# Kernel tuning notes

Measured on AMD Instinct MI355X. Metric: run time of the kernel, lower is better.

Reference implementation:

```python
import jax, jax.numpy as jnp
import numpy as np

B, S, T, I, H = 256, 128, 64, 63, 1024


def setup_inputs() -> dict:
    key = jax.random.key(0)
    ks = jax.random.split(key, 12)
    sc = 1.0 / np.sqrt(H)

    def rn(k, shape, scale=1.0):
        return jax.random.normal(k, shape, dtype=jnp.float32) * scale

    return dict(
        encoder_inputs=rn(ks[0], (B, S, I)),
        decoder_inputs=rn(ks[1], (B, T, I)),
        # encoder GRU params (PyTorch layout: [3H, in], gate order r,z,n)
        enc_Wih=rn(ks[2], (3 * H, I), sc), enc_Whh=rn(ks[3], (3 * H, H), sc),
        enc_bih=rn(ks[4], (3 * H,), sc), enc_bhh=rn(ks[5], (3 * H,), sc),
        # decoder GRUCell params (input dim = I, see notes)
        dec_Wih=rn(ks[6], (3 * H, I), sc), dec_Whh=rn(ks[7], (3 * H, H), sc),
        dec_bih=rn(ks[8], (3 * H,), sc), dec_bhh=rn(ks[9], (3 * H,), sc),
        # projector Linear(H -> I)
        proj_W=rn(ks[10], (I, H), sc), proj_b=rn(ks[11], (I,), sc),
    )


def _gru_gates(gi, gh, h):
    # gi = W_ih x + b_ih, gh = W_hh h + b_hh; PyTorch gate order (r, z, n)
    i_r, i_z, i_n = jnp.split(gi, 3, axis=-1)
    h_r, h_z, h_n = jnp.split(gh, 3, axis=-1)
    r = jax.nn.sigmoid(i_r + h_r)
    z = jax.nn.sigmoid(i_z + h_z)
    n = jnp.tanh(i_n + r * h_n)
    return (1.0 - z) * n + z * h


def reference(encoder_inputs, decoder_inputs, enc_Wih, enc_Whh, enc_bih,
              enc_bhh, dec_Wih, dec_Whh, dec_bih, dec_bhh, proj_W, proj_b):
    hid = enc_Whh.shape[1]
    b = encoder_inputs.shape[0]
    # ---- encoder GRU (batch_first), input-side gates precomputed as one GEMM
    gi_all = jnp.einsum('bsi,gi->bsg', encoder_inputs, enc_Wih) + enc_bih  # (B,S,3H)

    def step(h, gi):
        gh = h @ enc_Whh.T + enc_bhh
        return _gru_gates(gi, gh, h), None

    h0 = jnp.zeros((b, hid), encoder_inputs.dtype)
    enc_h, _ = jax.lax.scan(step, h0, jnp.swapaxes(gi_all, 0, 1))  # (B,H) final hidden

    # ---- decoder: per the source, every timestep feeds the SAME encoder
    # hidden state into the GRUCell (state is not carried), so all timesteps
    # are independent and can be computed as batched GEMMs over (B,T).
    gi_dec = jnp.einsum('bti,gi->btg', decoder_inputs, dec_Wih) + dec_bih   # (B,T,3H)
    gh_dec = (enc_h @ dec_Whh.T + dec_bhh)[:, None, :]                       # (B,1,3H)
    next_states = _gru_gates(gi_dec, gh_dec, enc_h[:, None, :])              # (B,T,H)

    # dropout p=0.0 (identity); projector Linear
    outputs = jnp.einsum('bth,oh->bto', next_states, proj_W) + proj_b       # (B,T,I)
    return outputs
```

## Files before the change

### kernel.cpp

```cpp
#include <hip/hip_runtime.h>


typedef unsigned short u16;
typedef unsigned int   u32;
typedef __attribute__((ext_vector_type(8))) short s8v;
typedef __attribute__((ext_vector_type(4))) float f4v;
typedef __attribute__((ext_vector_type(4))) int  i4v;
typedef __attribute__((ext_vector_type(4))) unsigned int u4v;

__device__ __forceinline__ float b2f(u16 u) {
    return __uint_as_float(((u32)u) << 16);
}
__device__ __forceinline__ u16 f2b(float f) {
    u32 x = __float_as_uint(f);
    u32 r = x + 0x7fffu + ((x >> 16) & 1u);
    return (u16)(r >> 16);
}
__device__ __forceinline__ float sigf(float x) {
    return 1.0f / (1.0f + __expf(-x));
}
__device__ __forceinline__ f4v mfma16(s8v a, s8v b, f4v c) {
    return __builtin_amdgcn_mfma_f32_16x16x32_bf16(a, b, c, 0, 0, 0);
}
__device__ __forceinline__ void unpack8(u4v w0, u4v w1, s8v& hi, s8v& lo) {
    u32 c0 = w0[0], c1 = w0[1], c2 = w0[2], c3 = w0[3];
    u32 c4 = w1[0], c5 = w1[1], c6 = w1[2], c7 = w1[3];
    union { u32 u[4]; s8v v; } H, L;
    H.u[0] = (c0 & 0xffffu) | (c1 << 16);
    H.u[1] = (c2 & 0xffffu) | (c3 << 16);
    H.u[2] = (c4 & 0xffffu) | (c5 << 16);
    H.u[3] = (c6 & 0xffffu) | (c7 << 16);
    L.u[0] = (c0 >> 16) | (c1 & 0xffff0000u);
    L.u[1] = (c2 >> 16) | (c3 & 0xffff0000u);
    L.u[2] = (c4 >> 16) | (c5 & 0xffff0000u);
    L.u[3] = (c6 >> 16) | (c7 & 0xffff0000u);
    hi = H.v; lo = L.v;
}

__global__ void zero_ws(i4v* __restrict__ p, int n) {
    int i = blockIdx.x * blockDim.x + threadIdx.x;
    if (i < n) { i4v z = {0, 0, 0, 0}; p[i] = z; }
}

__global__ void conv_wih_split_pad(const float* __restrict__ s,
                                   u16* __restrict__ hi, u16* __restrict__ lo) {
    int idx = blockIdx.x * blockDim.x + threadIdx.x;
    int row = idx >> 6, col = idx & 63;
    float v = (col < 63) ? s[(size_t)row * 63 + col] : 0.f;
    u16 h = f2b(v);
    hi[idx] = h;
    lo[idx] = f2b(v - b2f(h));
}

__global__ void conv_pw_split_pad(const float* __restrict__ s,
                                  u16* __restrict__ hi, u16* __restrict__ lo) {
    int idx = blockIdx.x * blockDim.x + threadIdx.x;
    float v = (idx < 63 * 1024) ? s[idx] : 0.f;
    u16 h = f2b(v);
    hi[idx] = h;
    lo[idx] = f2b(v - b2f(h));
}

__global__ __launch_bounds__(512, 1) void enc_persist8(
    const float* __restrict__ Whh,
    const u16* __restrict__ WihH, const u16* __restrict__ WihL,
    const float* __restrict__ bih, const float* __restrict__ bhh,
    const float* __restrict__ xenc,
    u32* __restrict__ hbuf,
    int* __restrict__ ep)
{
    __shared__ f4v red[8][4][3][64];
    __shared__ u16 WisH[48 * 72];
    __shared__ u16 WisL[48 * 72];

    __builtin_amdgcn_fence(__ATOMIC_ACQUIRE, "agent");

    const int tid  = threadIdx.x;
    const int lane = tid & 63;
    const int wave = tid >> 6;
    const int lrow = lane & 15;
    const int lk8  = lane >> 4;
    const int bid = blockIdx.x;
    const int xcd = bid & 7;
    const int y   = bid >> 3;
    const int mt  = y & 3;
    const int jt  = xcd * 8 + (y >> 2);
    const int m0 = mt * 64;
    const int j0 = jt * 16;

    int* subCtr  = ep + (mt * 8 + xcd) * 16;
    int* waveCtr = ep + (mt * 8 + wave) * 16;

    if (tid < 192) {
        int wr = tid >> 2, qq = tid & 3;
        int grow = (wr >> 4) * 1024 + j0 + (wr & 15);
        const u16* wpH = WihH + (size_t)grow * 64 + qq * 16;
        const u16* wpL = WihL + (size_t)grow * 64 + qq * 16;
        *(i4v*)&WisH[wr * 72 + qq * 16]     = *(const i4v*)wpH;
        *(i4v*)&WisH[wr * 72 + qq * 16 + 8] = *(const i4v*)(wpH + 8);
        *(i4v*)&WisL[wr * 72 + qq * 16]     = *(const i4v*)wpL;
        *(i4v*)&WisL[wr * 72 + qq * 16 + 8] = *(const i4v*)(wpL + 8);
    }

    s8v bHf[3][4], bLf[3][4];
    const int k0 = wave * 128;
    #pragma unroll
    for (int gg = 0; gg < 3; ++gg)
        #pragma unroll
        for (int ks = 0; ks < 4; ++ks) {
            const float* p = Whh + (size_t)(gg * 1024 + j0 + lrow) * 1024 +
                             k0 + ks * 32 + lk8 * 8;
            f4v a = *(const f4v*)p;
            f4v b = *(const f4v*)(p + 4);
            union { u16 a[8]; s8v v; } H, L;
            #pragma unroll
            for (int j = 0; j < 8; ++j) {
                float v = (j < 4) ? a[j] : b[j - 4];
                u16 hh = f2b(v);
                H.a[j] = hh;
                L.a[j] = f2b(v - b2f(hh));
            }
            bHf[gg][ks] = H.v;
            bLf[gg][ks] = L.v;
        }

    const int jcol = j0 + lrow;
    const float bhr = bhh[jcol], bhz = bhh[1024 + jcol], bhn = bhh[2048 + jcol];
    const float bir = bih[jcol], biz = bih[1024 + jcol], bin = bih[2048 + jcol];

    size_t aoff[4];
    #pragma unroll
    for (int mtile = 0; mtile < 4; ++mtile)
        aoff[mtile] = (size_t)(m0 + mtile * 16 + lrow) * 1024 + k0 + lk8 * 8;

    const float* xrow = xenc + (size_t)(m0 + (wave & 3) * 16 + lrow) * 8064;
    float hprev[4] = {0.f, 0.f, 0.f, 0.f};

    float xf[16];
    if (wave < 4) {
        #pragma unroll
        for (int ks = 0; ks < 2; ++ks)
            #pragma unroll
            for (int j = 0; j < 8; ++j) {
                int col = ks * 32 + lk8 * 8 + j;
                xf[ks * 8 + j] = (col < 63) ? xrow[col] : 0.f;
            }
    }

    __syncthreads();

    for (int s = 0; s < 128; ++s) {
        const u32* hin = hbuf + (size_t)s * 262144;
        u32* hout      = hbuf + (size_t)(s + 1) * 262144;

        f4v gi_r = {0.f, 0.f, 0.f, 0.f};
        f4v gi_z = {0.f, 0.f, 0.f, 0.f};
        f4v gi_n = {0.f, 0.f, 0.f, 0.f};
        if (wave < 4) {
            #pragma unroll
            for (int ks = 0; ks < 2; ++ks) {
                union { u16 a[8]; s8v v; } xh, xl;
                #pragma unroll
                for (int j = 0; j < 8; ++j) {
                    float v = xf[ks * 8 + j];
                    u16 hh = f2b(v);
                    xh.a[j] = hh;
                    xl.a[j] = f2b(v - b2f(hh));
                }
                int ao = ks * 32 + lk8 * 8;
                s8v brh = *(const s8v*)&WisH[(lrow) * 72 + ao];
                s8v brl = *(const s8v*)&WisL[(lrow) * 72 + ao];
                s8v bzh = *(const s8v*)&WisH[(16 + lrow) * 72 + ao];
                s8v bzl = *(const s8v*)&WisL[(16 + lrow) * 72 + ao];
                s8v bnh = *(const s8v*)&WisH[(32 + lrow) * 72 + ao];
                s8v bnl = *(const s8v*)&WisL[(32 + lrow) * 72 + ao];
                gi_r = mfma16(xh.v, brh, gi_r);
                gi_r = mfma16(xh.v, brl, gi_r);
                gi_r = mfma16(xl.v, brh, gi_r);
                gi_z = mfma16(xh.v, bzh, gi_z);
                gi_z = mfma16(xh.v, bzl, gi_z);
                gi_z = mfma16(xl.v, bzh, gi_z);
                gi_n = mfma16(xh.v, bnh, gi_n);
                gi_n = mfma16(xh.v, bnl, gi_n);
                gi_n = mfma16(xl.v, bnh, gi_n);
            }
        }

        if (s) {
            const int tgt = s * 8;
            while (__hip_atomic_load(waveCtr, __ATOMIC_RELAXED,
                                     __HIP_MEMORY_SCOPE_SYSTEM) < tgt)
                __builtin_amdgcn_s_sleep(1);
        }

        f4v accr[4], accz[4], acchn[4];
        #pragma unroll
        for (int m = 0; m < 4; ++m) {
            accr[m]  = f4v{0.f, 0.f, 0.f, 0.f};
            accz[m]  = f4v{0.f, 0.f, 0.f, 0.f};
            acchn[m] = f4v{0.f, 0.f, 0.f, 0.f};
        }
        #pragma unroll
        for (int mtile = 0; mtile < 4; ++mtile) {
            #pragma unroll
            for (int ks = 0; ks < 4; ++ks) {
                const u32* p = hin + aoff[mtile] + ks * 32;
                u4v w0 = *(const u4v*)p;
                u4v w1 = *(const u4v*)(p + 4);
                s8v ahi, alo;
                unpack8(w0, w1, ahi, alo);
                accr[mtile]  = mfma16(ahi, bHf[0][ks], accr[mtile]);
                accr[mtile]  = mfma16(ahi, bLf[0][ks], accr[mtile]);
                accr[mtile]  = mfma16(alo, bHf[0][ks], accr[mtile]);
                accz[mtile]  = mfma16(ahi, bHf[1][ks], accz[mtile]);
                accz[mtile]  = mfma16(ahi, bLf[1][ks], accz[mtile]);
                accz[mtile]  = mfma16(alo, bHf[1][ks], accz[mtile]);
                acchn[mtile] = mfma16(ahi, bHf[2][ks], acchn[mtile]);
                acchn[mtile] = mfma16(ahi, bLf[2][ks], acchn[mtile]);
                acchn[mtile] = mfma16(alo, bHf[2][ks], acchn[mtile]);
            }
        }

        #pragma unroll
        for (int m = 0; m < 4; ++m) {
            red[wave][m][0][lane] = accr[m];
            red[wave][m][1][lane] = accz[m];
            red[wave][m][2][lane] = acchn[m];
        }
        __syncthreads();

        if (wave < 4) {
            f4v sr = {0.f, 0.f, 0.f, 0.f};
            f4v sz = {0.f, 0.f, 0.f, 0.f};
            f4v sh = {0.f, 0.f, 0.f, 0.f};
            #pragma unroll
            for (int w = 0; w < 8; ++w) {
                sr += red[w][wave][0][lane];
                sz += red[w][wave][1][lane];
                sh += red[w][wave][2][lane];
            }
            #pragma unroll
            for (int reg = 0; reg < 4; ++reg) {
                int brow = m0 + wave * 16 + lk8 * 4 + reg;
                float rr = sigf(sr[reg] + gi_r[reg] + bir + bhr);
                float zz = sigf(sz[reg] + gi_z[reg] + biz + bhz);
                float nn = tanhf(gi_n[reg] + bin + rr * (sh[reg] + bhn));
                float h = (1.f - zz) * nn + zz * hprev[reg];
                u16 hh = f2b(h);
                u16 ll = f2b(h - b2f(hh));
                hprev[reg] = b2f(hh) + b2f(ll);
                u32 pk = (u32)hh | ((u32)ll << 16);
                __hip_atomic_store(&hout[(size_t)brow * 1024 + jcol], pk,
                                   __ATOMIC_RELAXED, __HIP_MEMORY_SCOPE_SYSTEM);
            }
        }

        __syncthreads();
        if (tid == 0)
            __hip_atomic_fetch_add(subCtr, 1, __ATOMIC_RELAXED,
                                   __HIP_MEMORY_SCOPE_SYSTEM);
        if (wave < 4) {
            int sn = (s < 127) ? s + 1 : 127;
            const float* xr = xrow + sn * 63;
            #pragma unroll
            for (int ks = 0; ks < 2; ++ks)
                #pragma unroll
                for (int j = 0; j < 8; ++j) {
                    int col = ks * 32 + lk8 * 8 + j;
                    xf[ks * 8 + j] = (col < 63) ? xr[col] : 0.f;
                }
        }
    }
}

__global__ __launch_bounds__(256, 1) void gru_gemm1(
    const float* __restrict__ Whh,
    const float* __restrict__ bhh,
    const u32* __restrict__ hin,
    float* __restrict__ gh_out)
{
    __shared__ u16 WbH[48 * 264];
    __shared__ u16 WbL[48 * 264];

    const int tid  = threadIdx.x;
    const int lane = tid & 63;
    const int wave = tid >> 6;
    const int lrow = lane & 15;
    const int lk8  = lane >> 4;
    const int mt = blockIdx.x & 3;
    const int jt = blockIdx.x >> 2;
    const int m0 = mt * 64;
    const int j0 = jt * 16;

    f4v acc_r  = {0.f, 0.f, 0.f, 0.f};
    f4v acc_z  = {0.f, 0.f, 0.f, 0.f};
    f4v acc_hn = {0.f, 0.f, 0.f, 0.f};

    f4v stgA[6], stgB[6];
    #pragma unroll
    for (int i = 0; i < 6; ++i) {
        int c16 = i * 256 + tid;
        int row = c16 >> 5, p16 = c16 & 31;
        int grow = (row >> 4) * 1024 + j0 + (row & 15);
        const float* p = Whh + (size_t)grow * 1024 + p16 * 8;
        stgA[i] = *(const f4v*)p;
        stgB[i] = *(const f4v*)(p + 4);
    }
    #pragma unroll
    for (int i = 0; i < 6; ++i) {
        int c16 = i * 256 + tid;
        int row = c16 >> 5, p16 = c16 & 31;
        union { u16 a[8]; i4v v; } H, L;
        #pragma unroll
        for (int j = 0; j < 8; ++j) {
            float v = (j < 4) ? stgA[i][j] : stgB[i][j - 4];
            u16 hh = f2b(v);
            H.a[j] = hh;
            L.a[j] = f2b(v - b2f(hh));
        }
        *(i4v*)&WbH[row * 264 + p16 * 8] = H.v;
        *(i4v*)&WbL[row * 264 + p16 * 8] = L.v;
    }
    __syncthreads();

    const size_t arow = (size_t)(m0 + wave * 16 + lrow) * 1024 + lk8 * 8;
    const u32* hp = hin + arow;

    for (int c = 0; c < 4; ++c) {
        if (c < 3) {
            #pragma unroll
            for (int i = 0; i < 6; ++i) {
                int c16 = i * 256 + tid;
                int row = c16 >> 5, p16 = c16 & 31;
                int grow = (row >> 4) * 1024 + j0 + (row & 15);
                const float* p = Whh + (size_t)grow * 1024 + (c + 1) * 256 + p16 * 8;
                stgA[i] = *(const f4v*)p;
                stgB[i] = *(const f4v*)(p + 4);
            }
        }
        #pragma unroll
        for (int ks = 0; ks < 8; ++ks) {
            int kk = c * 256 + ks * 32;
            int bo = ks * 32 + lk8 * 8;
            u4v w0 = *(const u4v*)(hp + kk);
            u4v w1 = *(const u4v*)(hp + kk + 4);
            s8v ahi, alo;
            unpack8(w0, w1, ahi, alo);
            s8v brh = *(const s8v*)&WbH[(lrow) * 264 + bo];
            s8v brl = *(const s8v*)&WbL[(lrow) * 264 + bo];
            s8v bzh = *(const s8v*)&WbH[(16 + lrow) * 264 + bo];
            s8v bzl = *(const s8v*)&WbL[(16 + lrow) * 264 + bo];
            s8v bnh = *(const s8v*)&WbH[(32 + lrow) * 264 + bo];
            s8v bnl = *(const s8v*)&WbL[(32 + lrow) * 264 + bo];
            acc_r  = mfma16(ahi, brh, acc_r);
            acc_r  = mfma16(ahi, brl, acc_r);
            acc_r  = mfma16(alo, brh, acc_r);
            acc_z  = mfma16(ahi, bzh, acc_z);
            acc_z  = mfma16(ahi, bzl, acc_z);
            acc_z  = mfma16(alo, bzh, acc_z);
            acc_hn = mfma16(ahi, bnh, acc_hn);
            acc_hn = mfma16(ahi, bnl, acc_hn);
            acc_hn = mfma16(alo, bnh, acc_hn);
        }
        __syncthreads();
        if (c < 3) {
            #pragma unroll
            for (int i = 0; i < 6; ++i) {
                int c16 = i * 256 + tid;
                int row = c16 >> 5, p16 = c16 & 31;
                union { u16 a[8]; i4v v; } H, L;
                #pragma unroll
                for (int j = 0; j < 8; ++j) {
                    float v = (j < 4) ? stgA[i][j] : stgB[i][j - 4];
                    u16 hh = f2b(v);
                    H.a[j] = hh;
                    L.a[j] = f2b(v - b2f(hh));
                }
                *(i4v*)&WbH[row * 264 + p16 * 8] = H.v;
                *(i4v*)&WbL[row * 264 + p16 * 8] = L.v;
            }
            __syncthreads();
        }
    }

    const int jcol = j0 + lrow;
    const float bhr = bhh[jcol];
    const float bhz = bhh[1024 + jcol];
    const float bhn = bhh[2048 + jcol];
    #pragma unroll
    for (int reg = 0; reg < 4; ++reg) {
        int brow = m0 + wave * 16 + lk8 * 4 + reg;
        gh_out[(size_t)brow * 3072 + jcol]        = acc_r[reg] + bhr;
        gh_out[(size_t)brow * 3072 + 1024 + jcol] = acc_z[reg] + bhz;
        gh_out[(size_t)brow * 3072 + 2048 + jcol] = acc_hn[reg] + bhn;
    }
}

__global__ __launch_bounds__(256, 1) void dec_fused(
    const u16* __restrict__ WihH, const u16* __restrict__ WihL,
    const float* __restrict__ bih,
    const float* __restrict__ xdec,
    const u32* __restrict__ e32,
    const float* __restrict__ gh,
    const u16* __restrict__ pWH, const u16* __restrict__ pWL,
    const float* __restrict__ pb,
    float* __restrict__ out)
{
    __shared__ u16 XdH[64 * 72];
    __shared__ u16 XdL[64 * 72];
    __shared__ u16 WiH_[192 * 72];
    __shared__ u16 WiL_[192 * 72];
    __shared__ u16 nsH[64 * 72];
    __shared__ u16 nsL[64 * 72];

    const int tid  = threadIdx.x;
    const int lane = tid & 63;
    const int wave = tid >> 6;
    const int lrow = lane & 15;
    const int lk8  = lane >> 4;
    const int b    = blockIdx.x;

    {
        int row = tid >> 2, q = tid & 3;
        const float* xr = xdec + (size_t)(b * 64 + row) * 63;
        #pragma unroll
        for (int ii = 0; ii < 16; ++ii) {
            int col = q * 16 + ii;
            float v = (col < 63) ? xr[col] : 0.f;
            u16 hh = f2b(v);
            XdH[row * 72 + col] = hh;
            XdL[row * 72 + col] = f2b(v - b2f(hh));
        }
    }

    f4v oacc[4];
    #pragma unroll
    for (int f = 0; f < 4; ++f) oacc[f] = f4v{0.f, 0.f, 0.f, 0.f};

    for (int j0 = 0; j0 < 1024; j0 += 64) {
        #pragma unroll
        for (int k = 0; k < 3; ++k) {
            int c = tid + k * 256;
            int r = c >> 2, qq = c & 3;
            int grow = (r >> 6) * 1024 + j0 + (r & 63);
            const u16* srcH = WihH + (size_t)grow * 64 + qq * 16;
            const u16* srcL = WihL + (size_t)grow * 64 + qq * 16;
            *(i4v*)&WiH_[r * 72 + qq * 16]     = *(const i4v*)srcH;
            *(i4v*)&WiH_[r * 72 + qq * 16 + 8] = *(const i4v*)(srcH + 8);
            *(i4v*)&WiL_[r * 72 + qq * 16]     = *(const i4v*)srcL;
            *(i4v*)&WiL_[r * 72 + qq * 16 + 8] = *(const i4v*)(srcL + 8);
        }
        __syncthreads();

        f4v ar[4], az[4], an[4];
        #pragma unroll
        for (int jf = 0; jf < 4; ++jf) {
            ar[jf] = f4v{0.f, 0.f, 0.f, 0.f};
            az[jf] = f4v{0.f, 0.f, 0.f, 0.f};
            an[jf] = f4v{0.f, 0.f, 0.f, 0.f};
        }
        #pragma unroll
        for (int ks = 0; ks < 2; ++ks) {
            int ao = ks * 32 + lk8 * 8;
            s8v ah = *(const s8v*)&XdH[(wave * 16 + lrow) * 72 + ao];
            s8v al = *(const s8v*)&XdL[(wave * 16 + lrow) * 72 + ao];
            #pragma unroll
            for (int jf = 0; jf < 4; ++jf) {
                s8v brh = *(const s8v*)&WiH_[(jf * 16 + lrow) * 72 + ao];
                s8v brl = *(const s8v*)&WiL_[(jf * 16 + lrow) * 72 + ao];
                s8v bzh = *(const s8v*)&WiH_[(64 + jf * 16 + lrow) * 72 + ao];
                s8v bzl = *(const s8v*)&WiL_[(64 + jf * 16 + lrow) * 72 + ao];
                s8v bnh = *(const s8v*)&WiH_[(128 + jf * 16 + lrow) * 72 + ao];
                s8v bnl = *(const s8v*)&WiL_[(128 + jf * 16 + lrow) * 72 + ao];
                ar[jf] = mfma16(ah, brh, ar[jf]);
                ar[jf] = mfma16(ah, brl, ar[jf]);
                ar[jf] = mfma16(al, brh, ar[jf]);
                az[jf] = mfma16(ah, bzh, az[jf]);
                az[jf] = mfma16(ah, bzl, az[jf]);
                az[jf] = mfma16(al, bzh, az[jf]);
                an[jf] = mfma16(ah, bnh, an[jf]);
                an[jf] = mfma16(ah, bnl, an[jf]);
                an[jf] = mfma16(al, bnh, an[jf]);
            }
        }

        #pragma unroll
        for (int jf = 0; jf < 4; ++jf) {
            int j = j0 + jf * 16 + lrow;
            float ghr = gh[(size_t)b * 3072 + j];
            float ghz = gh[(size_t)b * 3072 + 1024 + j];
            float ghn = gh[(size_t)b * 3072 + 2048 + j];
            float bir = bih[j];
            float biz = bih[1024 + j];
            float bin = bih[2048 + j];
            u32 pk = e32[(size_t)b * 1024 + j];
            float he = b2f((u16)(pk & 0xffffu)) + b2f((u16)(pk >> 16));
            #pragma unroll
            for (int reg = 0; reg < 4; ++reg) {
                float r  = sigf(ar[jf][reg] + bir + ghr);
                float z  = sigf(az[jf][reg] + biz + ghz);
                float nn = tanhf(an[jf][reg] + bin + r * ghn);
                float v  = (1.f - z) * nn + z * he;
                u16 hh = f2b(v);
                int lo_i = (wave * 16 + lk8 * 4 + reg) * 72 + jf * 16 + lrow;
                nsH[lo_i] = hh;
                nsL[lo_i] = f2b(v - b2f(hh));
            }
        }
        __syncthreads();

        #pragma unroll
        for (int ks = 0; ks < 2; ++ks) {
            int ao = ks * 32 + lk8 * 8;
            s8v ah = *(const s8v*)&nsH[(wave * 16 + lrow) * 72 + ao];
            s8v al = *(const s8v*)&nsL[(wave * 16 + lrow) * 72 + ao];
            #pragma unroll
            for (int f = 0; f < 4; ++f) {
                size_t bo = (size_t)(f * 16 + lrow) * 1024 + j0 + ks * 32 + lk8 * 8;
                s8v bh = *(const s8v*)(pWH + bo);
                s8v bl = *(const s8v*)(pWL + bo);
                oacc[f] = mfma16(ah, bh, oacc[f]);
                oacc[f] = mfma16(ah, bl, oacc[f]);
                oacc[f] = mfma16(al, bh, oacc[f]);
            }
        }
        __syncthreads();
    }

    #pragma unroll
    for (int f = 0; f < 4; ++f) {
        int o = f * 16 + lrow;
        if (o < 63) {
            float pbv = pb[o];
            #pragma unroll
            for (int reg = 0; reg < 4; ++reg) {
                int t = wave * 16 + lk8 * 4 + reg;
                out[((size_t)(b * 64 + t)) * 63 + o] = oacc[f][reg] + pbv;
            }
        }
    }
}

extern "C" void kernel_launch(void* const* d_in, const int* in_sizes, int n_in,
                              void* d_out, int out_size, void* d_ws, size_t ws_size,
                              hipStream_t stream)
{
    const float* enc_x = (const float*)d_in[0];
    const float* dec_x = (const float*)d_in[1];
    const float* eWih  = (const float*)d_in[2];
    const float* eWhh  = (const float*)d_in[3];
    const float* ebih  = (const float*)d_in[4];
    const float* ebhh  = (const float*)d_in[5];
    const float* dWih  = (const float*)d_in[6];
    const float* dWhh  = (const float*)d_in[7];
    const float* dbih  = (const float*)d_in[8];
    const float* dbhh  = (const float*)d_in[9];
    const float* pW    = (const float*)d_in[10];
    const float* pb    = (const float*)d_in[11];

    char* ws = (char*)d_ws;

    u32*   hbuf  = (u32*)(ws);
    int*   ep    = (int*)(ws + 135266304);
    float* ghd   = (float*)(ws + 135282688);
    u16*   eWihH = (u16*)(ws + 138428416);
    u16*   eWihL = (u16*)(ws + 138821632);
    u16*   dWihH = (u16*)(ws + 139214848);
    u16*   dWihL = (u16*)(ws + 139608064);
    u16*   pWH   = (u16*)(ws + 140001280);
    u16*   pWL   = (u16*)(ws + 140132352);

    conv_wih_split_pad<<<dim3(768), dim3(256), 0, stream>>>(eWih, eWihH, eWihL);
    conv_wih_split_pad<<<dim3(768), dim3(256), 0, stream>>>(dWih, dWihH, dWihL);
    conv_pw_split_pad<<<dim3(256), dim3(256), 0, stream>>>(pW, pWH, pWL);

    zero_ws<<<dim3(256), dim3(256), 0, stream>>>((i4v*)hbuf, 65536);
    zero_ws<<<dim3(4), dim3(256), 0, stream>>>((i4v*)ep, 1024);

    enc_persist8<<<dim3(256), dim3(512), 0, stream>>>(
        eWhh, eWihH, eWihL, ebih, ebhh, enc_x, hbuf, ep);

    u32* Hfin = hbuf + (size_t)128 * 262144;

    gru_gemm1<<<dim3(256), dim3(256), 0, stream>>>(dWhh, dbhh, Hfin, ghd);

    dec_fused<<<dim3(256), dim3(256), 0, stream>>>(
        dWihH, dWihL, dbih, dec_x, Hfin, ghd, pWH, pWL, pb, (float*)d_out);
}
```

Before: 1.520 ms.

## Split encoder batch into two sub-tiles with separate counters; store hidden hi/lo planes

Each encoder block now processes two 32-row batch sub-tiles, each with its own progress counter. The second sub-tile's wait and GEMM can overlap with the first sub-tile's finalize and publication, and each sub-tile signals as soon as its own waves finish storing rather than after a block-wide barrier. The hidden state is stored as separate bf16 hi and lo planes instead of packed u32, which removes the unpack step in the encoder, gemm1 and the decoder. MFMA issue order is interleaved across the r, z and n gates to shorten dependency chains. The cost is more synchronisation points, two 16-bit atomic stores per element, and a changed counter target that has to match the new signalling scheme.

```diff
diff --git a/kernel.cpp b/kernel.cpp
--- a/kernel.cpp
+++ b/kernel.cpp
@@ -6,7 +6,6 @@
 typedef __attribute__((ext_vector_type(8))) short s8v;
 typedef __attribute__((ext_vector_type(4))) float f4v;
 typedef __attribute__((ext_vector_type(4))) int  i4v;
-typedef __attribute__((ext_vector_type(4))) unsigned int u4v;
 
 __device__ __forceinline__ float b2f(u16 u) {
     return __uint_as_float(((u32)u) << 16);
@@ -21,20 +20,6 @@
 }
 __device__ __forceinline__ f4v mfma16(s8v a, s8v b, f4v c) {
     return __builtin_amdgcn_mfma_f32_16x16x32_bf16(a, b, c, 0, 0, 0);
-}
-__device__ __forceinline__ void unpack8(u4v w0, u4v w1, s8v& hi, s8v& lo) {
-    u32 c0 = w0[0], c1 = w0[1], c2 = w0[2], c3 = w0[3];
-    u32 c4 = w1[0], c5 = w1[1], c6 = w1[2], c7 = w1[3];
-    union { u32 u[4]; s8v v; } H, L;
-    H.u[0] = (c0 & 0xffffu) | (c1 << 16);
-    H.u[1] = (c2 & 0xffffu) | (c3 << 16);
-    H.u[2] = (c4 & 0xffffu) | (c5 << 16);
-    H.u[3] = (c6 & 0xffffu) | (c7 << 16);
-    L.u[0] = (c0 >> 16) | (c1 & 0xffff0000u);
-    L.u[1] = (c2 >> 16) | (c3 & 0xffff0000u);
-    L.u[2] = (c4 >> 16) | (c5 & 0xffff0000u);
-    L.u[3] = (c6 >> 16) | (c7 & 0xffff0000u);
-    hi = H.v; lo = L.v;
 }
 
 __global__ void zero_ws(i4v* __restrict__ p, int n) {
@@ -61,15 +46,16 @@
     lo[idx] = f2b(v - b2f(h));
 }
 
-__global__ __launch_bounds__(512, 1) void enc_persist8(
+__global__ __launch_bounds__(512, 1) void enc_persist9(
     const float* __restrict__ Whh,
     const u16* __restrict__ WihH, const u16* __restrict__ WihL,
     const float* __restrict__ bih, const float* __restrict__ bhh,
     const float* __restrict__ xenc,
-    u32* __restrict__ hbuf,
+    u16* __restrict__ hbufH, u16* __restrict__ hbufL,
     int* __restrict__ ep)
 {
-    __shared__ f4v red[8][4][3][64];
+    __shared__ f4v redA[8][2][3][64];
+    __shared__ f4v redB[8][2][3][64];
     __shared__ u16 WisH[48 * 72];
     __shared__ u16 WisL[48 * 72];
 
@@ -83,13 +69,18 @@
     const int bid = blockIdx.x;
     const int xcd = bid & 7;
     const int y   = bid >> 3;
-    const int mt  = y & 3;
+    const int p   = y & 3;
     const int jt  = xcd * 8 + (y >> 2);
-    const int m0 = mt * 64;
-    const int j0 = jt * 16;
-
-    int* subCtr  = ep + (mt * 8 + xcd) * 16;
-    int* waveCtr = ep + (mt * 8 + wave) * 16;
+    const int j0  = jt * 16;
+    const int mtA = p;
+    const int mtB = p + 4;
+    const int mA  = mtA * 32;
+    const int mB  = mtB * 32;
+
+    int* subCtrA  = ep + (mtA * 8 + xcd) * 16;
+    int* subCtrB  = ep + (mtB * 8 + xcd) * 16;
+    int* waveCtrA = ep + (mtA * 8 + wave) * 16;
+    int* waveCtrB = ep + (mtB * 8 + wave) * 16;
 
     if (tid < 192) {
         int wr = tid >> 2, qq = tid & 3;
@@ -108,10 +99,10 @@
     for (int gg = 0; gg < 3; ++gg)
         #pragma unroll
         for (int ks = 0; ks < 4; ++ks) {
-            const float* p = Whh + (size_t)(gg * 1024 + j0 + lrow) * 1024 +
-                             k0 + ks * 32 + lk8 * 8;
-            f4v a = *(const f4v*)p;
-            f4v b = *(const f4v*)(p + 4);
+            const float* ptr = Whh + (size_t)(gg * 1024 + j0 + lrow) * 1024 +
+                               k0 + ks * 32 + lk8 * 8;
+            f4v a = *(const f4v*)ptr;
+            f4v b = *(const f4v*)(ptr + 4);
             union { u16 a[8]; s8v v; } H, L;
             #pragma unroll
             for (int j = 0; j < 8; ++j) {
@@ -128,12 +119,17 @@
     const float bhr = bhh[jcol], bhz = bhh[1024 + jcol], bhn = bhh[2048 + jcol];
     const float bir = bih[jcol], biz = bih[1024 + jcol], bin = bih[2048 + jcol];
 
-    size_t aoff[4];
+    size_t aoffA[2], aoffB[2];
     #pragma unroll
-    for (int mtile = 0; mtile < 4; ++mtile)
-        aoff[mtile] = (size_t)(m0 + mtile * 16 + lrow) * 1024 + k0 + lk8 * 8;
-
-    const float* xrow = xenc + (size_t)(m0 + (wave & 3) * 16 + lrow) * 8064;
+    for (int t = 0; t < 2; ++t) {
+        aoffA[t] = (size_t)(mA + t * 16 + lrow) * 1024 + k0 + lk8 * 8;
+        aoffB[t] = (size_t)(mB + t * 16 + lrow) * 1024 + k0 + lk8 * 8;
+    }
+
+    const int egrp = (wave >> 1) & 1;
+    const int wl   = wave & 1;
+    const int myM  = (egrp ? mB : mA) + wl * 16;
+    const float* xrow = xenc + (size_t)(myM + lrow) * 8064;
     float hprev[4] = {0.f, 0.f, 0.f, 0.f};
 
     float xf[16];
@@ -150,8 +146,10 @@
     __syncthreads();
 
     for (int s = 0; s < 128; ++s) {
-        const u32* hin = hbuf + (size_t)s * 262144;
-        u32* hout      = hbuf + (size_t)(s + 1) * 262144;
+        const u16* hinH = hbufH + (size_t)s * 262144;
+        const u16* hinL = hbufL + (size_t)s * 262144;
+        u16* houtH = hbufH + (size_t)(s + 1) * 262144;
+        u16* houtL = hbufL + (size_t)(s + 1) * 262144;
 
         f4v gi_r = {0.f, 0.f, 0.f, 0.f};
         f4v gi_z = {0.f, 0.f, 0.f, 0.f};
@@ -175,73 +173,69 @@
                 s8v bnh = *(const s8v*)&WisH[(32 + lrow) * 72 + ao];
                 s8v bnl = *(const s8v*)&WisL[(32 + lrow) * 72 + ao];
                 gi_r = mfma16(xh.v, brh, gi_r);
+                gi_z = mfma16(xh.v, bzh, gi_z);
+                gi_n = mfma16(xh.v, bnh, gi_n);
                 gi_r = mfma16(xh.v, brl, gi_r);
+                gi_z = mfma16(xh.v, bzl, gi_z);
+                gi_n = mfma16(xh.v, bnl, gi_n);
                 gi_r = mfma16(xl.v, brh, gi_r);
-                gi_z = mfma16(xh.v, bzh, gi_z);
-                gi_z = mfma16(xh.v, bzl, gi_z);
                 gi_z = mfma16(xl.v, bzh, gi_z);
-                gi_n = mfma16(xh.v, bnh, gi_n);
-                gi_n = mfma16(xh.v, bnl, gi_n);
                 gi_n = mfma16(xl.v, bnh, gi_n);
             }
         }
 
         if (s) {
-            const int tgt = s * 8;
-            while (__hip_atomic_load(waveCtr, __ATOMIC_RELAXED,
+            const int tgt = 16 * s;
+            while (__hip_atomic_load(waveCtrA, __ATOMIC_RELAXED,
                                      __HIP_MEMORY_SCOPE_SYSTEM) < tgt)
                 __builtin_amdgcn_s_sleep(1);
         }
-
-        f4v accr[4], accz[4], acchn[4];
-        #pragma unroll
-        for (int m = 0; m < 4; ++m) {
-            accr[m]  = f4v{0.f, 0.f, 0.f, 0.f};
-            accz[m]  = f4v{0.f, 0.f, 0.f, 0.f};
-            acchn[m] = f4v{0.f, 0.f, 0.f, 0.f};
-        }
-        #pragma unroll
-        for (int mtile = 0; mtile < 4; ++mtile) {
-            #pragma unroll
-            for (int ks = 0; ks < 4; ++ks) {
-                const u32* p = hin + aoff[mtile] + ks * 32;
-                u4v w0 = *(const u4v*)p;
-                u4v w1 = *(const u4v*)(p + 4);
-                s8v ahi, alo;
-                unpack8(w0, w1, ahi, alo);
-                accr[mtile]  = mfma16(ahi, bHf[0][ks], accr[mtile]);
-                accr[mtile]  = mfma16(ahi, bLf[0][ks], accr[mtile]);
-                accr[mtile]  = mfma16(alo, bHf[0][ks], accr[mtile]);
-                accz[mtile]  = mfma16(ahi, bHf[1][ks], accz[mtile]);
-                accz[mtile]  = mfma16(ahi, bLf[1][ks], accz[mtile]);
-                accz[mtile]  = mfma16(alo, bHf[1][ks], accz[mtile]);
-                acchn[mtile] = mfma16(ahi, bHf[2][ks], acchn[mtile]);
-                acchn[mtile] = mfma16(ahi, bLf[2][ks], acchn[mtile]);
-                acchn[mtile] = mfma16(alo, bHf[2][ks], acchn[mtile]);
-            }
-        }
-
-        #pragma unroll
-        for (int m = 0; m < 4; ++m) {
-            red[wave][m][0][lane] = accr[m];
-            red[wave][m][1][lane] = accz[m];
-            red[wave][m][2][lane] = acchn[m];
+        {
+            f4v ar[2], az[2], ah[2];
+            #pragma unroll
+            for (int t = 0; t < 2; ++t) {
+                ar[t] = f4v{0.f, 0.f, 0.f, 0.f};
+                az[t] = f4v{0.f, 0.f, 0.f, 0.f};
+                ah[t] = f4v{0.f, 0.f, 0.f, 0.f};
+            }
+            #pragma unroll
+            for (int t = 0; t < 2; ++t)
+                #pragma unroll
+                for (int ks = 0; ks < 4; ++ks) {
+                    s8v ahi = *(const s8v*)(hinH + aoffA[t] + ks * 32);
+                    s8v alo = *(const s8v*)(hinL + aoffA[t] + ks * 32);
+                    ar[t] = mfma16(ahi, bHf[0][ks], ar[t]);
+                    az[t] = mfma16(ahi, bHf[1][ks], az[t]);
+                    ah[t] = mfma16(ahi, bHf[2][ks], ah[t]);
+                    ar[t] = mfma16(ahi, bLf[0][ks], ar[t]);
+                    az[t] = mfma16(ahi, bLf[1][ks], az[t]);
+                    ah[t] = mfma16(ahi, bLf[2][ks], ah[t]);
+                    ar[t] = mfma16(alo, bHf[0][ks], ar[t]);
+                    az[t] = mfma16(alo, bHf[1][ks], az[t]);
+                    ah[t] = mfma16(alo, bHf[2][ks], ah[t]);
+                }
+            #pragma unroll
+            for (int t = 0; t < 2; ++t) {
+                redA[wave][t][0][lane] = ar[t];
+                redA[wave][t][1][lane] = az[t];
+                redA[wave][t][2][lane] = ah[t];
+            }
         }
         __syncthreads();
 
-        if (wave < 4) {
+        if (wave < 2) {
             f4v sr = {0.f, 0.f, 0.f, 0.f};
             f4v sz = {0.f, 0.f, 0.f, 0.f};
             f4v sh = {0.f, 0.f, 0.f, 0.f};
             #pragma unroll
             for (int w = 0; w < 8; ++w) {
-                sr += red[w][wave][0][lane];
-                sz += red[w][wave][1][lane];
-                sh += red[w][wave][2][lane];
+                sr += redA[w][wl][0][lane];
+                sz += redA[w][wl][1][lane];
+                sh += redA[w][wl][2][lane];
             }
             #pragma unroll
             for (int reg = 0; reg < 4; ++reg) {
-                int brow = m0 + wave * 16 + lk8 * 4 + reg;
+                int brow = mA + wl * 16 + lk8 * 4 + reg;
                 float rr = sigf(sr[reg] + gi_r[reg] + bir + bhr);
                 float zz = sigf(sz[reg] + gi_z[reg] + biz + bhz);
                 float nn = tanhf(gi_n[reg] + bin + rr * (sh[reg] + bhn));
@@ -249,16 +243,89 @@
                 u16 hh = f2b(h);
                 u16 ll = f2b(h - b2f(hh));
                 hprev[reg] = b2f(hh) + b2f(ll);
-                u32 pk = (u32)hh | ((u32)ll << 16);
-                __hip_atomic_store(&hout[(size_t)brow * 1024 + jcol], pk,
-                                   __ATOMIC_RELAXED, __HIP_MEMORY_SCOPE_SYSTEM);
-            }
-        }
-
+                size_t off = (size_t)brow * 1024 + jcol;
+                __hip_atomic_store(&houtH[off], hh, __ATOMIC_RELAXED,
+                                   __HIP_MEMORY_SCOPE_SYSTEM);
+                __hip_atomic_store(&houtL[off], ll, __ATOMIC_RELAXED,
+                                   __HIP_MEMORY_SCOPE_SYSTEM);
+            }
+            asm volatile("s_waitcnt vmcnt(0)" ::: "memory");
+            if (lane == 0)
+                __hip_atomic_fetch_add(subCtrA, 1, __ATOMIC_RELAXED,
+                                       __HIP_MEMORY_SCOPE_SYSTEM);
+        }
+
+        if (s) {
+            const int tgt = 16 * s;
+            while (__hip_atomic_load(waveCtrB, __ATOMIC_RELAXED,
+                                     __HIP_MEMORY_SCOPE_SYSTEM) < tgt)
+                __builtin_amdgcn_s_sleep(1);
+        }
+        {
+            f4v ar[2], az[2], ah[2];
+            #pragma unroll
+            for (int t = 0; t < 2; ++t) {
+                ar[t] = f4v{0.f, 0.f, 0.f, 0.f};
+                az[t] = f4v{0.f, 0.f, 0.f, 0.f};
+                ah[t] = f4v{0.f, 0.f, 0.f, 0.f};
+            }
+            #pragma unroll
+            for (int t = 0; t < 2; ++t)
+                #pragma unroll
+                for (int ks = 0; ks < 4; ++ks) {
+                    s8v ahi = *(const s8v*)(hinH + aoffB[t] + ks * 32);
+                    s8v alo = *(const s8v*)(hinL + aoffB[t] + ks * 32);
+                    ar[t] = mfma16(ahi, bHf[0][ks], ar[t]);
+                    az[t] = mfma16(ahi, bHf[1][ks], az[t]);
+                    ah[t] = mfma16(ahi, bHf[2][ks], ah[t]);
+                    ar[t] = mfma16(ahi, bLf[0][ks], ar[t]);
+                    az[t] = mfma16(ahi, bLf[1][ks], az[t]);
+                    ah[t] = mfma16(ahi, bLf[2][ks], ah[t]);
+                    ar[t] = mfma16(alo, bHf[0][ks], ar[t]);
+                    az[t] = mfma16(alo, bHf[1][ks], az[t]);
+                    ah[t] = mfma16(alo, bHf[2][ks], ah[t]);
+                }
+            #pragma unroll
+            for (int t = 0; t < 2; ++t) {
+                redB[wave][t][0][lane] = ar[t];
+                redB[wave][t][1][lane] = az[t];
+                redB[wave][t][2][lane] = ah[t];
+            }
+        }
         __syncthreads();
-        if (tid == 0)
-            __hip_atomic_fetch_add(subCtr, 1, __ATOMIC_RELAXED,
+
+        if (wave >= 2 && wave < 4) {
+            f4v sr = {0.f, 0.f, 0.f, 0.f};
+            f4v sz = {0.f, 0.f, 0.f, 0.f};
+            f4v sh = {0.f, 0.f, 0.f, 0.f};
+            #pragma unroll
+            for (int w = 0; w < 8; ++w) {
+                sr += redB[w][wl][0][lane];
+                sz += redB[w][wl][1][lane];
+                sh += redB[w][wl][2][lane];
+            }
+            #pragma unroll
+            for (int reg = 0; reg < 4; ++reg) {
+                int brow = mB + wl * 16 + lk8 * 4 + reg;
+                float rr = sigf(sr[reg] + gi_r[reg] + bir + bhr);
+                float zz = sigf(sz[reg] + gi_z[reg] + biz + bhz);
+                float nn = tanhf(gi_n[reg] + bin + rr * (sh[reg] + bhn));
+                float h = (1.f - zz) * nn + zz * hprev[reg];
+                u16 hh = f2b(h);
+                u16 ll = f2b(h - b2f(hh));
+                hprev[reg] = b2f(hh) + b2f(ll);
+                size_t off = (size_t)brow * 1024 + jcol;
+                __hip_atomic_store(&houtH[off], hh, __ATOMIC_RELAXED,
                                    __HIP_MEMORY_SCOPE_SYSTEM);
+                __hip_atomic_store(&houtL[off], ll, __ATOMIC_RELAXED,
+                                   __HIP_MEMORY_SCOPE_SYSTEM);
+            }
+            asm volatile("s_waitcnt vmcnt(0)" ::: "memory");
+            if (lane == 0)
+                __hip_atomic_fetch_add(subCtrB, 1, __ATOMIC_RELAXED,
+                                       __HIP_MEMORY_SCOPE_SYSTEM);
+        }
+
         if (wave < 4) {
             int sn = (s < 127) ? s + 1 : 127;
             const float* xr = xrow + sn * 63;
@@ -276,7 +343,7 @@
 __global__ __launch_bounds__(256, 1) void gru_gemm1(
     const float* __restrict__ Whh,
     const float* __restrict__ bhh,
-    const u32* __restrict__ hin,
+    const u16* __restrict__ hinH, const u16* __restrict__ hinL,
     float* __restrict__ gh_out)
 {
     __shared__ u16 WbH[48 * 264];
@@ -324,7 +391,8 @@
     __syncthreads();
 
     const size_t arow = (size_t)(m0 + wave * 16 + lrow) * 1024 + lk8 * 8;
-    const u32* hp = hin + arow;
+    const u16* hp = hinH + arow;
+    const u16* lp = hinL + arow;
 
     for (int c = 0; c < 4; ++c) {
         if (c < 3) {
@@ -342,10 +410,8 @@
         for (int ks = 0; ks < 8; ++ks) {
             int kk = c * 256 + ks * 32;
             int bo = ks * 32 + lk8 * 8;
-            u4v w0 = *(const u4v*)(hp + kk);
-            u4v w1 = *(const u4v*)(hp + kk + 4);
-            s8v ahi, alo;
-            unpack8(w0, w1, ahi, alo);
+            s8v ahi = *(const s8v*)(hp + kk);
+            s8v alo = *(const s8v*)(lp + kk);
             s8v brh = *(const s8v*)&WbH[(lrow) * 264 + bo];
             s8v brl = *(const s8v*)&WbL[(lrow) * 264 + bo];
             s8v bzh = *(const s8v*)&WbH[(16 + lrow) * 264 + bo];
@@ -353,13 +419,13 @@
             s8v bnh = *(const s8v*)&WbH[(32 + lrow) * 264 + bo];
             s8v bnl = *(const s8v*)&WbL[(32 + lrow) * 264 + bo];
             acc_r  = mfma16(ahi, brh, acc_r);
+            acc_z  = mfma16(ahi, bzh, acc_z);
+            acc_hn = mfma16(ahi, bnh, acc_hn);
             acc_r  = mfma16(ahi, brl, acc_r);
+            acc_z  = mfma16(ahi, bzl, acc_z);
+            acc_hn = mfma16(ahi, bnl, acc_hn);
             acc_r  = mfma16(alo, brh, acc_r);
-            acc_z  = mfma16(ahi, bzh, acc_z);
-            acc_z  = mfma16(ahi, bzl, acc_z);
             acc_z  = mfma16(alo, bzh, acc_z);
-            acc_hn = mfma16(ahi, bnh, acc_hn);
-            acc_hn = mfma16(ahi, bnl, acc_hn);
             acc_hn = mfma16(alo, bnh, acc_hn);
         }
         __syncthreads();
@@ -400,7 +466,7 @@
     const u16* __restrict__ WihH, const u16* __restrict__ WihL,
     const float* __restrict__ bih,
     const float* __restrict__ xdec,
-    const u32* __restrict__ e32,
+    const u16* __restrict__ ehi, const u16* __restrict__ elo,
     const float* __restrict__ gh,
     const u16* __restrict__ pWH, const u16* __restrict__ pWL,
     const float* __restrict__ pb,
@@ -473,13 +539,13 @@
                 s8v bnh = *(const s8v*)&WiH_[(128 + jf * 16 + lrow) * 72 + ao];
                 s8v bnl = *(const s8v*)&WiL_[(128 + jf * 16 + lrow) * 72 + ao];
                 ar[jf] = mfma16(ah, brh, ar[jf]);
+                az[jf] = mfma16(ah, bzh, az[jf]);
+                an[jf] = mfma16(ah, bnh, an[jf]);
                 ar[jf] = mfma16(ah, brl, ar[jf]);
+                az[jf] = mfma16(ah, bzl, az[jf]);
+                an[jf] = mfma16(ah, bnl, an[jf]);
                 ar[jf] = mfma16(al, brh, ar[jf]);
-                az[jf] = mfma16(ah, bzh, az[jf]);
-                az[jf] = mfma16(ah, bzl, az[jf]);
                 az[jf] = mfma16(al, bzh, az[jf]);
-                an[jf] = mfma16(ah, bnh, an[jf]);
-                an[jf] = mfma16(ah, bnl, an[jf]);
                 an[jf] = mfma16(al, bnh, an[jf]);
             }
         }
@@ -493,8 +559,8 @@
             float bir = bih[j];
             float biz = bih[1024 + j];
             float bin = bih[2048 + j];
-            u32 pk = e32[(size_t)b * 1024 + j];
-            float he = b2f((u16)(pk & 0xffffu)) + b2f((u16)(pk >> 16));
+            size_t eo = (size_t)b * 1024 + j;
+            float he = b2f(ehi[eo]) + b2f(elo[eo]);
             #pragma unroll
             for (int reg = 0; reg < 4; ++reg) {
                 float r  = sigf(ar[jf][reg] + bir + ghr);
@@ -560,7 +626,8 @@
 
     char* ws = (char*)d_ws;
 
-    u32*   hbuf  = (u32*)(ws);
+    u16*   hbufH = (u16*)(ws);
+    u16*   hbufL = (u16*)(ws + 67633152);
     int*   ep    = (int*)(ws + 135266304);
     float* ghd   = (float*)(ws + 135282688);
     u16*   eWihH = (u16*)(ws + 138428416);
@@ -574,16 +641,19 @@
     conv_wih_split_pad<<<dim3(768), dim3(256), 0, stream>>>(dWih, dWihH, dWihL);
     conv_pw_split_pad<<<dim3(256), dim3(256), 0, stream>>>(pW, pWH, pWL);
 
-    zero_ws<<<dim3(256), dim3(256), 0, stream>>>((i4v*)hbuf, 65536);
+    zero_ws<<<dim3(128), dim3(256), 0, stream>>>((i4v*)hbufH, 32768);
+    zero_ws<<<dim3(128), dim3(256), 0, stream>>>((i4v*)hbufL, 32768);
     zero_ws<<<dim3(4), dim3(256), 0, stream>>>((i4v*)ep, 1024);
 
-    enc_persist8<<<dim3(256), dim3(512), 0, stream>>>(
-        eWhh, eWihH, eWihL, ebih, ebhh, enc_x, hbuf, ep);
-
-    u32* Hfin = hbuf + (size_t)128 * 262144;
-
-    gru_gemm1<<<dim3(256), dim3(256), 0, stream>>>(dWhh, dbhh, Hfin, ghd);
+    enc_persist9<<<dim3(256), dim3(512), 0, stream>>>(
+        eWhh, eWihH, eWihL, ebih, ebhh, enc_x, hbufH, hbufL, ep);
+
+    u16* HfinH = hbufH + (size_t)128 * 262144;
+    u16* HfinL = hbufL + (size_t)128 * 262144;
+
+    gru_gemm1<<<dim3(256), dim3(256), 0, stream>>>(dWhh, dbhh, HfinH, HfinL, ghd);
 
     dec_fused<<<dim3(256), dim3(256), 0, stream>>>(
-        dWihH, dWihL, dbih, dec_x, Hfin, ghd, pWH, pWL, pb, (float*)d_out);
-}
+        dWihH, dWihL, dbih, dec_x, HfinH, HfinL, ghd, pWH, pWL, pb,
+        (float*)d_out);
+}
```

Measured after the change: 1.735 ms. 1.14x slower.

## Replace encoder step counters with NaN-sentinel polling on hidden-state data

Applied to the files above, without the earlier changes.

The persistent encoder no longer waits on per-wave atomic counters between timesteps. Instead the hidden-state buffers for steps 1..128 are pre-filled with a bf16 NaN sentinel, and readers spin (with sleep and cache-bypassing reloads) on each 16-byte chunk until the sentinel is overwritten. This removes the counter increments and the global barrier-style wait, letting each tile proceed as soon as its own input data arrives. The MFMA chains are also interleaved across the r/z/n accumulators to hide dependency latency. In exchange it adds a large sentinel fill pass over the hidden buffer, and it relies on the assumption that real data never exactly matches the sentinel pattern.

```diff
diff --git a/kernel.cpp b/kernel.cpp
--- a/kernel.cpp
+++ b/kernel.cpp
@@ -37,9 +37,28 @@
     hi = H.v; lo = L.v;
 }
 
+__device__ __forceinline__ u4v fix_chunk(const u32* p, u4v w) {
+    while (((w[0] >> 16) == 0x7FC0u) || ((w[1] >> 16) == 0x7FC0u) ||
+           ((w[2] >> 16) == 0x7FC0u) || ((w[3] >> 16) == 0x7FC0u)) {
+        __builtin_amdgcn_s_sleep(2);
+        unsigned long long a = (unsigned long long)p;
+        asm volatile("global_load_dwordx4 %0, %1, off sc0 sc1\n\t"
+                     "s_waitcnt vmcnt(0)"
+                     : "=&v"(w) : "v"(a) : "memory");
+    }
+    return w;
+}
+
 __global__ void zero_ws(i4v* __restrict__ p, int n) {
     int i = blockIdx.x * blockDim.x + threadIdx.x;
     if (i < n) { i4v z = {0, 0, 0, 0}; p[i] = z; }
+}
+
+__global__ void fill_sent(u4v* __restrict__ p, int n) {
+    int i = blockIdx.x * blockDim.x + threadIdx.x;
+    int st = gridDim.x * blockDim.x;
+    u4v s = {0x7FC07FC0u, 0x7FC07FC0u, 0x7FC07FC0u, 0x7FC07FC0u};
+    for (; i < n; i += st) p[i] = s;
 }
 
 __global__ void conv_wih_split_pad(const float* __restrict__ s,
@@ -61,13 +80,12 @@
     lo[idx] = f2b(v - b2f(h));
 }
 
-__global__ __launch_bounds__(512, 1) void enc_persist8(
+__global__ __launch_bounds__(512, 1) void enc_persist10(
     const float* __restrict__ Whh,
     const u16* __restrict__ WihH, const u16* __restrict__ WihL,
     const float* __restrict__ bih, const float* __restrict__ bhh,
     const float* __restrict__ xenc,
-    u32* __restrict__ hbuf,
-    int* __restrict__ ep)
+    u32* __restrict__ hbuf)
 {
     __shared__ f4v red[8][4][3][64];
     __shared__ u16 WisH[48 * 72];
@@ -87,9 +105,6 @@
     const int jt  = xcd * 8 + (y >> 2);
     const int m0 = mt * 64;
     const int j0 = jt * 16;
-
-    int* subCtr  = ep + (mt * 8 + xcd) * 16;
-    int* waveCtr = ep + (mt * 8 + wave) * 16;
 
     if (tid < 192) {
         int wr = tid >> 2, qq = tid & 3;
@@ -175,22 +190,15 @@
                 s8v bnh = *(const s8v*)&WisH[(32 + lrow) * 72 + ao];
                 s8v bnl = *(const s8v*)&WisL[(32 + lrow) * 72 + ao];
                 gi_r = mfma16(xh.v, brh, gi_r);
+                gi_z = mfma16(xh.v, bzh, gi_z);
+                gi_n = mfma16(xh.v, bnh, gi_n);
                 gi_r = mfma16(xh.v, brl, gi_r);
+                gi_z = mfma16(xh.v, bzl, gi_z);
+                gi_n = mfma16(xh.v, bnl, gi_n);
                 gi_r = mfma16(xl.v, brh, gi_r);
-                gi_z = mfma16(xh.v, bzh, gi_z);
-                gi_z = mfma16(xh.v, bzl, gi_z);
                 gi_z = mfma16(xl.v, bzh, gi_z);
-                gi_n = mfma16(xh.v, bnh, gi_n);
-                gi_n = mfma16(xh.v, bnl, gi_n);
                 gi_n = mfma16(xl.v, bnh, gi_n);
             }
-        }
-
-        if (s) {
-            const int tgt = s * 8;
-            while (__hip_atomic_load(waveCtr, __ATOMIC_RELAXED,
-                                     __HIP_MEMORY_SCOPE_SYSTEM) < tgt)
-                __builtin_amdgcn_s_sleep(1);
         }
 
         f4v accr[4], accz[4], acchn[4];
@@ -207,16 +215,18 @@
                 const u32* p = hin + aoff[mtile] + ks * 32;
                 u4v w0 = *(const u4v*)p;
                 u4v w1 = *(const u4v*)(p + 4);
+                w0 = fix_chunk(p, w0);
+                w1 = fix_chunk(p + 4, w1);
                 s8v ahi, alo;
                 unpack8(w0, w1, ahi, alo);
                 accr[mtile]  = mfma16(ahi, bHf[0][ks], accr[mtile]);
+                accz[mtile]  = mfma16(ahi, bHf[1][ks], accz[mtile]);
+                acchn[mtile] = mfma16(ahi, bHf[2][ks], acchn[mtile]);
                 accr[mtile]  = mfma16(ahi, bLf[0][ks], accr[mtile]);
+                accz[mtile]  = mfma16(ahi, bLf[1][ks], accz[mtile]);
+                acchn[mtile] = mfma16(ahi, bLf[2][ks], acchn[mtile]);
                 accr[mtile]  = mfma16(alo, bHf[0][ks], accr[mtile]);
-                accz[mtile]  = mfma16(ahi, bHf[1][ks], accz[mtile]);
-                accz[mtile]  = mfma16(ahi, bLf[1][ks], accz[mtile]);
                 accz[mtile]  = mfma16(alo, bHf[1][ks], accz[mtile]);
-                acchn[mtile] = mfma16(ahi, bHf[2][ks], acchn[mtile]);
-                acchn[mtile] = mfma16(ahi, bLf[2][ks], acchn[mtile]);
                 acchn[mtile] = mfma16(alo, bHf[2][ks], acchn[mtile]);
             }
         }
@@ -229,16 +239,20 @@
         }
         __syncthreads();
 
+        f4v sr = {0.f, 0.f, 0.f, 0.f};
+        f4v sz = {0.f, 0.f, 0.f, 0.f};
+        f4v sh = {0.f, 0.f, 0.f, 0.f};
         if (wave < 4) {
-            f4v sr = {0.f, 0.f, 0.f, 0.f};
-            f4v sz = {0.f, 0.f, 0.f, 0.f};
-            f4v sh = {0.f, 0.f, 0.f, 0.f};
             #pragma unroll
             for (int w = 0; w < 8; ++w) {
                 sr += red[w][wave][0][lane];
                 sz += red[w][wave][1][lane];
                 sh += red[w][wave][2][lane];
             }
+        }
+        __syncthreads();
+
+        if (wave < 4) {
             #pragma unroll
             for (int reg = 0; reg < 4; ++reg) {
                 int brow = m0 + wave * 16 + lk8 * 4 + reg;
@@ -253,13 +267,6 @@
                 __hip_atomic_store(&hout[(size_t)brow * 1024 + jcol], pk,
                                    __ATOMIC_RELAXED, __HIP_MEMORY_SCOPE_SYSTEM);
             }
-        }
-
-        __syncthreads();
-        if (tid == 0)
-            __hip_atomic_fetch_add(subCtr, 1, __ATOMIC_RELAXED,
-                                   __HIP_MEMORY_SCOPE_SYSTEM);
-        if (wave < 4) {
             int sn = (s < 127) ? s + 1 : 127;
             const float* xr = xrow + sn * 63;
             #pragma unroll
@@ -353,13 +360,13 @@
             s8v bnh = *(const s8v*)&WbH[(32 + lrow) * 264 + bo];
             s8v bnl = *(const s8v*)&WbL[(32 + lrow) * 264 + bo];
             acc_r  = mfma16(ahi, brh, acc_r);
+            acc_z  = mfma16(ahi, bzh, acc_z);
+            acc_hn = mfma16(ahi, bnh, acc_hn);
             acc_r  = mfma16(ahi, brl, acc_r);
+            acc_z  = mfma16(ahi, bzl, acc_z);
+            acc_hn = mfma16(ahi, bnl, acc_hn);
             acc_r  = mfma16(alo, brh, acc_r);
-            acc_z  = mfma16(ahi, bzh, acc_z);
-            acc_z  = mfma16(ahi, bzl, acc_z);
             acc_z  = mfma16(alo, bzh, acc_z);
-            acc_hn = mfma16(ahi, bnh, acc_hn);
-            acc_hn = mfma16(ahi, bnl, acc_hn);
             acc_hn = mfma16(alo, bnh, acc_hn);
         }
         __syncthreads();
@@ -473,13 +480,13 @@
                 s8v bnh = *(const s8v*)&WiH_[(128 + jf * 16 + lrow) * 72 + ao];
                 s8v bnl = *(const s8v*)&WiL_[(128 + jf * 16 + lrow) * 72 + ao];
                 ar[jf] = mfma16(ah, brh, ar[jf]);
+                az[jf] = mfma16(ah, bzh, az[jf]);
+                an[jf] = mfma16(ah, bnh, an[jf]);
                 ar[jf] = mfma16(ah, brl, ar[jf]);
+                az[jf] = mfma16(ah, bzl, az[jf]);
+                an[jf] = mfma16(ah, bnl, an[jf]);
                 ar[jf] = mfma16(al, brh, ar[jf]);
-                az[jf] = mfma16(ah, bzh, az[jf]);
-                az[jf] = mfma16(ah, bzl, az[jf]);
                 az[jf] = mfma16(al, bzh, az[jf]);
-                an[jf] = mfma16(ah, bnh, an[jf]);
-                an[jf] = mfma16(ah, bnl, an[jf]);
                 an[jf] = mfma16(al, bnh, an[jf]);
             }
         }
@@ -561,7 +568,6 @@
     char* ws = (char*)d_ws;
 
     u32*   hbuf  = (u32*)(ws);
-    int*   ep    = (int*)(ws + 135266304);
     float* ghd   = (float*)(ws + 135282688);
     u16*   eWihH = (u16*)(ws + 138428416);
     u16*   eWihL = (u16*)(ws + 138821632);
@@ -575,10 +581,11 @@
     conv_pw_split_pad<<<dim3(256), dim3(256), 0, stream>>>(pW, pWH, pWL);
 
     zero_ws<<<dim3(256), dim3(256), 0, stream>>>((i4v*)hbuf, 65536);
-    zero_ws<<<dim3(4), dim3(256), 0, stream>>>((i4v*)ep, 1024);
-
-    enc_persist8<<<dim3(256), dim3(512), 0, stream>>>(
-        eWhh, eWihH, eWihL, ebih, ebhh, enc_x, hbuf, ep);
+    fill_sent<<<dim3(4096), dim3(256), 0, stream>>>(
+        (u4v*)(hbuf + 262144), 8388608);
+
+    enc_persist10<<<dim3(256), dim3(512), 0, stream>>>(
+        eWhh, eWihH, eWihL, ebih, ebhh, enc_x, hbuf);
 
     u32* Hfin = hbuf + (size_t)128 * 262144;
 
```

Result: slower. 1.732 ms (+13.9%).
